# Kernel optimization log

Measured on AMD Instinct MI355X. Metric: run time of the kernel, lower is better.

## Reference

```python
import jax, jax.numpy as jnp
import numpy as np

N, F, H, E, R = 100000, 256, 64, 800000, 7
EPS = 1e-5

def _layernorm(x, g, b):
    mu = jnp.mean(x, axis=-1, keepdims=True)
    var = jnp.mean((x - mu) ** 2, axis=-1, keepdims=True)
    return (x - mu) * jax.lax.rsqrt(var + EPS) * g + b

def setup_inputs() -> dict:
    key = jax.random.key(0)
    ks = jax.random.split(key, 16)
    block_features = jax.random.normal(ks[0], (N, F), dtype=jnp.float32)
    src = jax.random.randint(ks[1], (E,), 0, N).astype(jnp.float32)
    dst = jax.random.randint(ks[2], (E,), 0, N).astype(jnp.float32)
    rel = jax.random.randint(ks[3], (E,), 0, R).astype(jnp.float32)
    w = jax.random.uniform(ks[4], (E,), dtype=jnp.float32)
    typed_edges = jnp.stack([src, dst, rel, w], axis=1)  # [E,4]
    def lin(k, fan_in, fan_out):
        s = 1.0 / np.sqrt(fan_in)
        k1, k2 = jax.random.split(k)
        return (jax.random.uniform(k1, (fan_in, fan_out), jnp.float32, -s, s),
                jax.random.uniform(k2, (fan_out,), jnp.float32, -s, s))
    W1, b1 = lin(ks[5], F, H)
    W2, b2 = lin(ks[6], H, H)
    rel_emb = jax.random.normal(ks[7], (R, H), dtype=jnp.float32)
    Wm1, bm1 = lin(ks[8], 3 * H + 1, H)
    Wm2, bm2 = lin(ks[9], H, H)
    Wg1, bg1 = lin(ks[10], 2 * H, H)
    Wg2, bg2 = lin(ks[11], H, H)
    return dict(block_features=block_features, typed_edges=typed_edges,
                W1=W1, b1=b1, g1=jnp.ones(H), be1=jnp.zeros(H), W2=W2, b2=b2,
                rel_emb=rel_emb, Wm1=Wm1, bm1=bm1, Wm2=Wm2, bm2=bm2,
                gn=jnp.ones(H), bn=jnp.zeros(H), Wg1=Wg1, bg1=bg1, Wg2=Wg2, bg2=bg2)

def reference(block_features, typed_edges, W1, b1, g1, be1, W2, b2, rel_emb,
              Wm1, bm1, Wm2, bm2, gn, bn, Wg1, bg1, Wg2, bg2):
    # node_proj: Linear -> LN -> ReLU -> Linear -> ReLU
    h = jax.nn.relu(_layernorm(block_features @ W1 + b1, g1, be1))
    h = jax.nn.relu(h @ W2 + b2)  # [N,H]
    src = typed_edges[:, 0].astype(jnp.int32)
    dst = typed_edges[:, 1].astype(jnp.int32)
    rel = typed_edges[:, 2].astype(jnp.int32)
    w = typed_edges[:, 3:4]  # [E,1]
    m_in = jnp.concatenate([h[src], h[dst], rel_emb[rel], w], axis=-1)  # [E,3H+1]
    msg = jax.nn.relu(m_in @ Wm1 + bm1) @ Wm2 + bm2  # [E,H]
    agg = jax.ops.segment_sum(msg, dst, num_segments=h.shape[0])  # [N,H]
    nodes = _layernorm(h + agg, gn, bn)
    g = jnp.concatenate([nodes.mean(axis=0), nodes.max(axis=0)], axis=-1)  # [2H]
    return jax.nn.relu(g @ Wg1 + bg1) @ Wg2 + bg2  # [H]
```

## Files before the change

### kernel.cpp

```cpp
#include <hip/hip_runtime.h>

typedef unsigned short u16;
typedef unsigned int   u32;
typedef __attribute__((ext_vector_type(8))) short bf16x8;
typedef __attribute__((ext_vector_type(4))) float f32x4;

#define EPS 1e-5f
#define MFMA(a,b,c) __builtin_amdgcn_mfma_f32_16x16x32_bf16(a,b,c,0,0,0)

constexpr int OB_b1=0, OB_g1=64, OB_be1=128, OB_b2=192, OB_bm1=256, OB_w192=320,
              OB_bm2=384, OB_gn=448, OB_bn=512, OB_bg1=576, OB_bg2=640,
              OB_Wg1=704, OB_Wg2=8896, WB_TOT=12992;
constexpr int FR_Wm1=0;
constexpr int FR_Wm2=12288;
constexpr int FR_rel=16384;
constexpr int FR_W1 =16960;
constexpr int FR_W2 =33344;
constexpr int FR_TOT=37440;

__device__ __forceinline__ float bf2f(u32 u) { return __uint_as_float(u << 16); }
__device__ __forceinline__ u16 f2bf(float f) {
  u32 b = __float_as_uint(f);
  return (u16)((b + 0x7fffu + ((b >> 16) & 1u)) >> 16);
}
__device__ __forceinline__ u32 fkey(float f) {
  u32 b = __float_as_uint(f);
  return (b & 0x80000000u) ? ~b : (b | 0x80000000u);
}

__launch_bounds__(256)
__global__ void k_prep(const float* __restrict__ W1, const float* __restrict__ b1,
                       const float* __restrict__ g1, const float* __restrict__ be1,
                       const float* __restrict__ W2, const float* __restrict__ b2,
                       const float* __restrict__ rel_emb,
                       const float* __restrict__ Wm1, const float* __restrict__ bm1,
                       const float* __restrict__ Wm2, const float* __restrict__ bm2,
                       const float* __restrict__ gn, const float* __restrict__ bn,
                       const float* __restrict__ Wg1, const float* __restrict__ bg1,
                       const float* __restrict__ Wg2, const float* __restrict__ bg2,
                       float* __restrict__ wbuf, u16* __restrict__ frags) {
  int tid = blockIdx.x * 256 + threadIdx.x;
  int nth = gridDim.x * 256;
  for (int i = tid; i < 64; i += nth) {
    wbuf[OB_b1 + i] = b1[i];   wbuf[OB_g1 + i] = g1[i];
    wbuf[OB_be1 + i] = be1[i]; wbuf[OB_b2 + i] = b2[i];
    wbuf[OB_bm1 + i] = bm1[i]; wbuf[OB_w192 + i] = Wm1[192 * 64 + i];
    wbuf[OB_bm2 + i] = bm2[i]; wbuf[OB_gn + i] = gn[i];
    wbuf[OB_bn + i] = bn[i];   wbuf[OB_bg1 + i] = bg1[i];
    wbuf[OB_bg2 + i] = bg2[i];
  }
  for (int i = tid; i < 8192; i += nth) wbuf[OB_Wg1 + i] = Wg1[i];
  for (int i = tid; i < 4096; i += nth) wbuf[OB_Wg2 + i] = Wg2[i];
  for (int idx = tid; idx < 16384; idx += nth) {
    int f = idx >> 9, L = (idx >> 3) & 63, j = idx & 7;
    int k = (f >> 2) * 32 + ((L >> 4) << 3) + j, n = ((f & 3) << 4) + (L & 15);
    frags[FR_W1 + idx] = f2bf(W1[k * 64 + n]);
  }
  for (int idx = tid; idx < 4096; idx += nth) {
    int f = idx >> 9, L = (idx >> 3) & 63, j = idx & 7;
    int k = (f >> 2) * 32 + ((L >> 4) << 3) + j, n = ((f & 3) << 4) + (L & 15);
    frags[FR_W2 + idx] = f2bf(W2[k * 64 + n]);
  }
  for (int idx = tid; idx < 12288; idx += nth) {
    int f = idx >> 9, L = (idx >> 3) & 63, j = idx & 7;
    int k = (f >> 2) * 32 + ((L >> 4) << 3) + j, n = ((f & 3) << 4) + (L & 15);
    frags[FR_Wm1 + idx] = f2bf(Wm1[k * 64 + n]);
  }
  for (int idx = tid; idx < 4096; idx += nth) {
    int f = idx >> 9, L = (idx >> 3) & 63, j = idx & 7;
    int k = (f >> 2) * 32 + ((L >> 4) << 3) + j, n = ((f & 3) << 4) + (L & 15);
    frags[FR_Wm2 + idx] = f2bf(Wm2[k * 64 + n]);
  }
  for (int idx = tid; idx < 576; idx += nth) {
    int r = idx / 80, c = idx % 80;
    frags[FR_rel + idx] = (r < 7 && c < 64) ? f2bf(rel_emb[r * 64 + c]) : (u16)0;
  }
}

__launch_bounds__(256, 3)
__global__ void k_h(const float* __restrict__ X, const float* __restrict__ wbuf,
                    const u16* __restrict__ frags, u16* __restrict__ hb, int N) {
  __shared__ __align__(16) u16 sW1[32 * 512];
  __shared__ __align__(16) u16 sW2[8 * 512];
  __shared__ __align__(16) u16 st[4][16 * 72];

  {
    const uint4* srcp = (const uint4*)(frags + FR_W1);
    uint4* d1 = (uint4*)sW1;
    for (int i = threadIdx.x; i < 2048; i += 256) d1[i] = srcp[i];
    const uint4* srcp2 = (const uint4*)(frags + FR_W2);
    uint4* d2 = (uint4*)sW2;
    for (int i = threadIdx.x; i < 512; i += 256) d2[i] = srcp2[i];
  }
  __syncthreads();

  int lane = threadIdx.x & 63, wave = threadIdx.x >> 6;
  int m = lane & 15, quad = lane >> 4, koff = quad * 8, col0 = m;

  float b1v[4], g1v[4], be1v[4], b2v[4];
  #pragma unroll
  for (int nt = 0; nt < 4; nt++) {
    int c = nt * 16 + col0;
    b1v[nt] = wbuf[OB_b1 + c]; g1v[nt] = wbuf[OB_g1 + c];
    be1v[nt] = wbuf[OB_be1 + c]; b2v[nt] = wbuf[OB_b2 + c];
  }

  int ntiles = (N + 15) / 16;
  int wid = blockIdx.x * 4 + wave, nw = gridDim.x * 4;
  for (int tile = wid; tile < ntiles; tile += nw) {
    int n0 = tile * 16;
    int nm = min(n0 + m, N - 1);
    const float* xr = X + (size_t)nm * 256 + koff;

    f32x4 acc[4] = {};
    #pragma unroll 1
    for (int ks = 0; ks < 8; ks++) {
      float4 u0 = *(const float4*)(xr + ks * 32);
      float4 u1 = *(const float4*)(xr + ks * 32 + 4);
      bf16x8 a;
      a[0] = (short)f2bf(u0.x); a[1] = (short)f2bf(u0.y);
      a[2] = (short)f2bf(u0.z); a[3] = (short)f2bf(u0.w);
      a[4] = (short)f2bf(u1.x); a[5] = (short)f2bf(u1.y);
      a[6] = (short)f2bf(u1.z); a[7] = (short)f2bf(u1.w);
      #pragma unroll
      for (int nt = 0; nt < 4; nt++) {
        bf16x8 b = *(const bf16x8*)(sW1 + (ks * 4 + nt) * 512 + lane * 8);
        acc[nt] = MFMA(a, b, acc[nt]);
      }
    }

    float v[4][4];
    #pragma unroll
    for (int nt = 0; nt < 4; nt++)
      #pragma unroll
      for (int r = 0; r < 4; r++) v[nt][r] = acc[nt][r] + b1v[nt];

    #pragma unroll
    for (int r = 0; r < 4; r++) {
      float s = v[0][r] + v[1][r] + v[2][r] + v[3][r];
      #pragma unroll
      for (int mk = 8; mk >= 1; mk >>= 1) s += __shfl_xor(s, mk, 64);
      float mu = s * (1.f / 64.f);
      float q = 0.f;
      #pragma unroll
      for (int nt = 0; nt < 4; nt++) { float d = v[nt][r] - mu; q += d * d; }
      #pragma unroll
      for (int mk = 8; mk >= 1; mk >>= 1) q += __shfl_xor(q, mk, 64);
      float rs = rsqrtf(q * (1.f / 64.f) + EPS);
      #pragma unroll
      for (int nt = 0; nt < 4; nt++) {
        float h1 = fmaxf(fmaf((v[nt][r] - mu) * rs, g1v[nt], be1v[nt]), 0.f);
        st[wave][(quad * 4 + r) * 72 + nt * 16 + col0] = f2bf(h1);
      }
    }
    __builtin_amdgcn_wave_barrier();

    f32x4 acc2[4] = {};
    #pragma unroll
    for (int ks = 0; ks < 2; ks++) {
      bf16x8 a2 = *(const bf16x8*)(st[wave] + m * 72 + ks * 32 + koff);
      #pragma unroll
      for (int nt = 0; nt < 4; nt++) {
        bf16x8 b = *(const bf16x8*)(sW2 + (ks * 4 + nt) * 512 + lane * 8);
        acc2[nt] = MFMA(a2, b, acc2[nt]);
      }
    }
    __builtin_amdgcn_wave_barrier();

    #pragma unroll
    for (int nt = 0; nt < 4; nt++)
      #pragma unroll
      for (int r = 0; r < 4; r++) {
        int row = n0 + quad * 4 + r;
        if (row < N)
          hb[(size_t)row * 64 + nt * 16 + col0] = f2bf(fmaxf(acc2[nt][r] + b2v[nt], 0.f));
      }
  }
}

__launch_bounds__(512, 6)
__global__ void k_edge(const float* __restrict__ te, const u16* __restrict__ hb,
                       const float* __restrict__ wbuf, const u16* __restrict__ frags,
                       float* __restrict__ agg, int E, int N) {
  __shared__ __align__(16) u16 sWm1[24 * 512];
  __shared__ __align__(16) u16 sWm2[8 * 512];
  __shared__ __align__(16) u16 srel[576];
  __shared__ __align__(16) u16 st[8][16 * 72];

  {
    const uint4* s1 = (const uint4*)(frags + FR_Wm1);
    uint4* d1 = (uint4*)sWm1;
    for (int i = threadIdx.x; i < 1536; i += 512) d1[i] = s1[i];
    const uint4* s2 = (const uint4*)(frags + FR_Wm2);
    uint4* d2 = (uint4*)sWm2;
    for (int i = threadIdx.x; i < 512; i += 512) d2[i] = s2[i];
    const uint4* s3 = (const uint4*)(frags + FR_rel);
    uint4* d3 = (uint4*)srel;
    for (int i = threadIdx.x; i < 72; i += 512) d3[i] = s3[i];
  }
  __syncthreads();

  int lane = threadIdx.x & 63, wave = threadIdx.x >> 6;
  int m = lane & 15, quad = lane >> 4, koff = quad * 8, col0 = m;

  float bm1v[4], w192v[4], bm2v[4];
  #pragma unroll
  for (int nt = 0; nt < 4; nt++) {
    int c = nt * 16 + col0;
    bm1v[nt] = wbuf[OB_bm1 + c];
    w192v[nt] = wbuf[OB_w192 + c];
    bm2v[nt] = wbuf[OB_bm2 + c];
  }

  int ntiles = (E + 15) / 16;
  int wid = blockIdx.x * 8 + wave, nw = gridDim.x * 8;

  int tile = wid;
  int src = 0, dstv = 0, rel = 0; float w = 0.f;
  bf16x8 af[6];

  if (tile < ntiles) {
    if (lane < 16) {
      int e = min(tile * 16 + lane, E - 1);
      float4 v = *(const float4*)(te + (size_t)e * 4);
      src  = min(max((int)v.x, 0), N - 1);
      dstv = min(max((int)v.y, 0), N - 1);
      rel  = min(max((int)v.z, 0), 6);
      w = v.w;
    }
    int sm = __shfl(src, m, 64), dm = __shfl(dstv, m, 64), rm = __shfl(rel, m, 64);
    const u16* hs = hb + (size_t)sm * 64;
    const u16* hd = hb + (size_t)dm * 64;
    af[0] = *(const bf16x8*)(hs + koff);
    af[1] = *(const bf16x8*)(hs + 32 + koff);
    af[2] = *(const bf16x8*)(hd + koff);
    af[3] = *(const bf16x8*)(hd + 32 + koff);
    af[4] = *(const bf16x8*)(srel + rm * 80 + koff);
    af[5] = *(const bf16x8*)(srel + rm * 80 + 32 + koff);
  }

  while (tile < ntiles) {
    int e0 = tile * 16;
    int tile_n = tile + nw;

    f32x4 acc[4] = {};
    #pragma unroll
    for (int ks = 0; ks < 6; ks++)
      #pragma unroll
      for (int nt = 0; nt < 4; nt++) {
        bf16x8 b = *(const bf16x8*)(sWm1 + (ks * 4 + nt) * 512 + lane * 8);
        acc[nt] = MFMA(af[ks], b, acc[nt]);
      }

    int dstc = dstv; float wc = w;

    if (tile_n < ntiles) {
      if (lane < 16) {
        int e = min(tile_n * 16 + lane, E - 1);
        float4 v = *(const float4*)(te + (size_t)e * 4);
        src  = min(max((int)v.x, 0), N - 1);
        dstv = min(max((int)v.y, 0), N - 1);
        rel  = min(max((int)v.z, 0), 6);
        w = v.w;
      }
      int sm = __shfl(src, m, 64), dm = __shfl(dstv, m, 64), rm = __shfl(rel, m, 64);
      const u16* hs = hb + (size_t)sm * 64;
      const u16* hd = hb + (size_t)dm * 64;
      af[0] = *(const bf16x8*)(hs + koff);
      af[1] = *(const bf16x8*)(hs + 32 + koff);
      af[2] = *(const bf16x8*)(hd + koff);
      af[3] = *(const bf16x8*)(hd + 32 + koff);
      af[4] = *(const bf16x8*)(srel + rm * 80 + koff);
      af[5] = *(const bf16x8*)(srel + rm * 80 + 32 + koff);
    }

    float wrow[4];
    #pragma unroll
    for (int r = 0; r < 4; r++) wrow[r] = __shfl(wc, quad * 4 + r, 64);
    #pragma unroll
    for (int nt = 0; nt < 4; nt++)
      #pragma unroll
      for (int r = 0; r < 4; r++) {
        float v = fmaf(wrow[r], w192v[nt], acc[nt][r] + bm1v[nt]);
        st[wave][(quad * 4 + r) * 72 + nt * 16 + col0] = f2bf(fmaxf(v, 0.f));
      }
    __builtin_amdgcn_wave_barrier();

    f32x4 acc2[4] = {};
    #pragma unroll
    for (int ks = 0; ks < 2; ks++) {
      bf16x8 a2 = *(const bf16x8*)(st[wave] + m * 72 + ks * 32 + koff);
      #pragma unroll
      for (int nt = 0; nt < 4; nt++) {
        bf16x8 b = *(const bf16x8*)(sWm2 + (ks * 4 + nt) * 512 + lane * 8);
        acc2[nt] = MFMA(a2, b, acc2[nt]);
      }
    }
    __builtin_amdgcn_wave_barrier();

    #pragma unroll
    for (int r = 0; r < 4; r++) {
      int row = quad * 4 + r;
      int dr = __shfl(dstc, row, 64);
      if (e0 + row < E) {
        #pragma unroll
        for (int nt = 0; nt < 4; nt++)
          atomicAdd(agg + (size_t)dr * 64 + nt * 16 + col0, acc2[nt][r] + bm2v[nt]);
      }
    }

    tile = tile_n;
  }
}

__launch_bounds__(256)
__global__ void k_nodes(const u16* __restrict__ hb, const float* __restrict__ agg,
                        const float* __restrict__ wbuf, float* __restrict__ gsum,
                        u32* __restrict__ gmax, int N) {
  int lane = threadIdx.x & 63, wave = threadIdx.x >> 6;
  int wid = blockIdx.x * 4 + wave;
  int nw = gridDim.x * 4;
  float gn = wbuf[OB_gn + lane], bn = wbuf[OB_bn + lane];
  float sj = 0.f, mj = -3.0e38f;
  for (int n = wid; n < N; n += nw) {
    float v = bf2f(hb[(size_t)n * 64 + lane]) + agg[(size_t)n * 64 + lane];
    float s = v;
    #pragma unroll
    for (int m = 32; m >= 1; m >>= 1) s += __shfl_xor(s, m, 64);
    float mu = s * (1.f / 64.f);
    float d = v - mu;
    float q = d * d;
    #pragma unroll
    for (int m = 32; m >= 1; m >>= 1) q += __shfl_xor(q, m, 64);
    float rs = rsqrtf(q * (1.f / 64.f) + EPS);
    float val = fmaf(d * rs, gn, bn);
    sj += val;
    mj = fmaxf(mj, val);
  }
  __shared__ float bs[256], bm[256];
  bs[threadIdx.x] = sj;
  bm[threadIdx.x] = mj;
  __syncthreads();
  if (threadIdx.x < 64) {
    int t = threadIdx.x;
    float ts = bs[t] + bs[64 + t] + bs[128 + t] + bs[192 + t];
    float tm = fmaxf(fmaxf(bm[t], bm[64 + t]), fmaxf(bm[128 + t], bm[192 + t]));
    atomicAdd(gsum + t, ts);
    atomicMax(gmax + t, fkey(tm));
  }
}

__launch_bounds__(128)
__global__ void k_final(const float* __restrict__ wbuf, const float* __restrict__ gsum,
                        const u32* __restrict__ gmax, float* __restrict__ out, int N) {
  __shared__ float g[128];
  __shared__ float y1[64];
  int t = threadIdx.x;
  if (t < 64) {
    g[t] = gsum[t] / (float)N;
  } else {
    u32 k = gmax[t - 64];
    u32 b = (k & 0x80000000u) ? (k & 0x7fffffffu) : ~k;
    g[t] = __uint_as_float(b);
  }
  __syncthreads();
  if (t < 64) {
    float a = wbuf[OB_bg1 + t];
    for (int i = 0; i < 128; i++) a = fmaf(g[i], wbuf[OB_Wg1 + i * 64 + t], a);
    y1[t] = fmaxf(a, 0.f);
  }
  __syncthreads();
  if (t < 64) {
    float a = wbuf[OB_bg2 + t];
    for (int k = 0; k < 64; k++) a = fmaf(y1[k], wbuf[OB_Wg2 + k * 64 + t], a);
    out[t] = a;
  }
}

extern "C" void kernel_launch(void* const* d_in, const int* in_sizes, int n_in,
                              void* d_out, int out_size, void* d_ws, size_t ws_size,
                              hipStream_t stream) {
  const int N = in_sizes[0] / 256;
  const int E = in_sizes[1] / 4;

  char* ws = (char*)d_ws;
  size_t aggB = (size_t)N * 64 * 4;
  size_t hbB  = (size_t)N * 64 * 2;
  float* agg   = (float*)ws;
  u16*   hb    = (u16*)(ws + aggB);
  float* gsum  = (float*)(ws + aggB + hbB);
  u32*   gmax  = (u32*)(ws + aggB + hbB + 256);
  float* wbuf  = (float*)(ws + aggB + hbB + 512);
  u16*   frags = (u16*)(ws + aggB + hbB + 512 + (size_t)WB_TOT * 4);

  const float* X  = (const float*)d_in[0];
  const float* te = (const float*)d_in[1];

  hipLaunchKernelGGL(k_prep, dim3(64), dim3(256), 0, stream,
                     (const float*)d_in[2], (const float*)d_in[3], (const float*)d_in[4],
                     (const float*)d_in[5], (const float*)d_in[6], (const float*)d_in[7],
                     (const float*)d_in[8], (const float*)d_in[9], (const float*)d_in[10],
                     (const float*)d_in[11], (const float*)d_in[12], (const float*)d_in[13],
                     (const float*)d_in[14], (const float*)d_in[15], (const float*)d_in[16],
                     (const float*)d_in[17], (const float*)d_in[18], wbuf, frags);
  hipMemsetAsync(agg, 0, aggB, stream);
  hipMemsetAsync(gsum, 0, 512, stream);
  hipLaunchKernelGGL(k_h, dim3(640), dim3(256), 0, stream, X, wbuf, frags, hb, N);
  hipLaunchKernelGGL(k_edge, dim3(768), dim3(512), 0, stream, te, hb, wbuf, frags, agg, E, N);
  hipLaunchKernelGGL(k_nodes, dim3(2048), dim3(256), 0, stream, hb, agg, wbuf, gsum, gmax, N);
  hipLaunchKernelGGL(k_final, dim3(1), dim3(128), 0, stream, wbuf, gsum, gmax, (float*)d_out, N);
}
```

Baseline: 452.1 us.

## Sort edges by destination with counting sort and fuse aggregation with node layernorm

Adds a histogram, a three-pass prefix scan and a scatter step that build a destination-sorted (CSR-like) edge list. The edge MLP kernel then assigns 64 destination nodes to each block, accumulates messages in shared memory instead of with global float atomics, and applies the node layernorm and global mean/max pooling in the same kernel. This removes the global agg buffer, its memset and the separate node kernel, at the cost of several extra launches, global atomics in the counting sort, an extra pass over the edges, and load imbalance across blocks with uneven in-degree.

```diff
diff --git a/kernel.cpp b/kernel.cpp
--- a/kernel.cpp
+++ b/kernel.cpp
@@ -77,6 +77,85 @@
   }
 }
 
+__launch_bounds__(256)
+__global__ void k_hist(const float* __restrict__ te, int* __restrict__ cnt, int E, int N) {
+  int i = blockIdx.x * 256 + threadIdx.x, st = gridDim.x * 256;
+  for (int e = i; e < E; e += st) {
+    float4 v = *(const float4*)(te + (size_t)e * 4);
+    int d = min(max((int)v.y, 0), N - 1);
+    atomicAdd(&cnt[d], 1);
+  }
+}
+
+#define SCH 512
+__launch_bounds__(256)
+__global__ void k_scan1(const int* __restrict__ cnt, int* __restrict__ bsum, int N) {
+  __shared__ int sd[256];
+  int b = blockIdx.x, t = threadIdx.x, base = b * SCH;
+  int i0 = base + 2 * t, i1 = i0 + 1;
+  int a = 0;
+  if (i0 < N) a += cnt[i0];
+  if (i1 < N) a += cnt[i1];
+  sd[t] = a; __syncthreads();
+  for (int s = 128; s > 0; s >>= 1) { if (t < s) sd[t] += sd[t + s]; __syncthreads(); }
+  if (t == 0) bsum[b] = sd[0];
+}
+
+__launch_bounds__(256)
+__global__ void k_scan2(const int* __restrict__ bsum, int* __restrict__ bofs,
+                        int* __restrict__ ofs, int NBLK, int N) {
+  __shared__ int sd[256];
+  int t = threadIdx.x;
+  int K = (NBLK + 255) / 256;
+  int loc = 0;
+  for (int k = 0; k < K; k++) { int i = t * K + k; if (i < NBLK) loc += bsum[i]; }
+  sd[t] = loc; __syncthreads();
+  for (int s = 1; s < 256; s <<= 1) {
+    int o = 0; if (t >= s) o = sd[t - s];
+    __syncthreads(); sd[t] += o; __syncthreads();
+  }
+  int excl = sd[t] - loc;
+  int run = excl;
+  for (int k = 0; k < K; k++) {
+    int i = t * K + k;
+    if (i < NBLK) { bofs[i] = run; run += bsum[i]; }
+  }
+  if (t == 255) ofs[N] = sd[255];
+}
+
+__launch_bounds__(256)
+__global__ void k_scan3(const int* __restrict__ bofs, int* __restrict__ ofs,
+                        int* __restrict__ cur, int N) {
+  __shared__ int sd[256];
+  int b = blockIdx.x, t = threadIdx.x, base = b * SCH;
+  int i0 = base + 2 * t, i1 = i0 + 1;
+  int a0 = (i0 < N) ? cur[i0] : 0, a1 = (i1 < N) ? cur[i1] : 0;
+  int pair = a0 + a1;
+  sd[t] = pair; __syncthreads();
+  for (int s = 1; s < 256; s <<= 1) {
+    int o = 0; if (t >= s) o = sd[t - s];
+    __syncthreads(); sd[t] += o; __syncthreads();
+  }
+  int excl = sd[t] - pair + bofs[b];
+  if (i0 < N) { ofs[i0] = excl;      cur[i0] = excl; }
+  if (i1 < N) { ofs[i1] = excl + a0; cur[i1] = excl + a0; }
+}
+
+__launch_bounds__(256)
+__global__ void k_place(const float* __restrict__ te, int* __restrict__ cur,
+                        uint4* __restrict__ sorted, int E, int N) {
+  int i = blockIdx.x * 256 + threadIdx.x, st = gridDim.x * 256;
+  for (int e = i; e < E; e += st) {
+    float4 v = *(const float4*)(te + (size_t)e * 4);
+    int s = min(max((int)v.x, 0), N - 1);
+    int d = min(max((int)v.y, 0), N - 1);
+    int r = min(max((int)v.z, 0), 6);
+    int pos = atomicAdd(&cur[d], 1);
+    uint4 rec; rec.x = (u32)s; rec.y = (u32)d; rec.z = (u32)r; rec.w = __float_as_uint(v.w);
+    sorted[pos] = rec;
+  }
+}
+
 __launch_bounds__(256, 3)
 __global__ void k_h(const float* __restrict__ X, const float* __restrict__ wbuf,
                     const u16* __restrict__ frags, u16* __restrict__ hb, int N) {
@@ -178,14 +257,19 @@
   }
 }
 
-__launch_bounds__(512, 6)
-__global__ void k_edge(const float* __restrict__ te, const u16* __restrict__ hb,
-                       const float* __restrict__ wbuf, const u16* __restrict__ frags,
-                       float* __restrict__ agg, int E, int N) {
+#define DPB 64
+#define APAD 68
+__launch_bounds__(512, 4)
+__global__ void k_edge_agg(const uint4* __restrict__ sorted, const u16* __restrict__ hb,
+                           const float* __restrict__ wbuf, const u16* __restrict__ frags,
+                           const int* __restrict__ ofs,
+                           float* __restrict__ gsum, u32* __restrict__ gmax, int N) {
   __shared__ __align__(16) u16 sWm1[24 * 512];
   __shared__ __align__(16) u16 sWm2[8 * 512];
   __shared__ __align__(16) u16 srel[576];
   __shared__ __align__(16) u16 st[8][16 * 72];
+  __shared__ float accum[DPB * APAD];
+  __shared__ float bs[512], bm[512];
 
   {
     const uint4* s1 = (const uint4*)(frags + FR_Wm1);
@@ -198,10 +282,15 @@
     uint4* d3 = (uint4*)srel;
     for (int i = threadIdx.x; i < 72; i += 512) d3[i] = s3[i];
   }
+  for (int i = threadIdx.x; i < DPB * APAD; i += 512) accum[i] = 0.f;
   __syncthreads();
 
   int lane = threadIdx.x & 63, wave = threadIdx.x >> 6;
   int m = lane & 15, quad = lane >> 4, koff = quad * 8, col0 = m;
+
+  int dlo = blockIdx.x * DPB;
+  int ndst = min(DPB, N - dlo);
+  int elo = ofs[dlo], ehi = ofs[dlo + ndst];
 
   float bm1v[4], w192v[4], bm2v[4];
   #pragma unroll
@@ -212,36 +301,26 @@
     bm2v[nt] = wbuf[OB_bm2 + c];
   }
 
-  int ntiles = (E + 15) / 16;
-  int wid = blockIdx.x * 8 + wave, nw = gridDim.x * 8;
-
-  int tile = wid;
-  int src = 0, dstv = 0, rel = 0; float w = 0.f;
-  bf16x8 af[6];
-
-  if (tile < ntiles) {
+  int ntile = (ehi - elo + 15) >> 4;
+  for (int ti = wave; ti < ntile; ti += 8) {
+    int e0 = elo + ti * 16;
+    int src = 0, dstv = 0, rel = 0; float w = 0.f;
     if (lane < 16) {
-      int e = min(tile * 16 + lane, E - 1);
-      float4 v = *(const float4*)(te + (size_t)e * 4);
-      src  = min(max((int)v.x, 0), N - 1);
-      dstv = min(max((int)v.y, 0), N - 1);
-      rel  = min(max((int)v.z, 0), 6);
-      w = v.w;
+      int e = min(e0 + lane, ehi - 1);
+      uint4 rc = sorted[e];
+      src = (int)rc.x; dstv = (int)rc.y; rel = (int)rc.z; w = __uint_as_float(rc.w);
     }
     int sm = __shfl(src, m, 64), dm = __shfl(dstv, m, 64), rm = __shfl(rel, m, 64);
+
     const u16* hs = hb + (size_t)sm * 64;
     const u16* hd = hb + (size_t)dm * 64;
+    bf16x8 af[6];
     af[0] = *(const bf16x8*)(hs + koff);
     af[1] = *(const bf16x8*)(hs + 32 + koff);
     af[2] = *(const bf16x8*)(hd + koff);
     af[3] = *(const bf16x8*)(hd + 32 + koff);
     af[4] = *(const bf16x8*)(srel + rm * 80 + koff);
     af[5] = *(const bf16x8*)(srel + rm * 80 + 32 + koff);
-  }
-
-  while (tile < ntiles) {
-    int e0 = tile * 16;
-    int tile_n = tile + nw;
 
     f32x4 acc[4] = {};
     #pragma unroll
@@ -252,31 +331,9 @@
         acc[nt] = MFMA(af[ks], b, acc[nt]);
       }
 
-    int dstc = dstv; float wc = w;
-
-    if (tile_n < ntiles) {
-      if (lane < 16) {
-        int e = min(tile_n * 16 + lane, E - 1);
-        float4 v = *(const float4*)(te + (size_t)e * 4);
-        src  = min(max((int)v.x, 0), N - 1);
-        dstv = min(max((int)v.y, 0), N - 1);
-        rel  = min(max((int)v.z, 0), 6);
-        w = v.w;
-      }
-      int sm = __shfl(src, m, 64), dm = __shfl(dstv, m, 64), rm = __shfl(rel, m, 64);
-      const u16* hs = hb + (size_t)sm * 64;
-      const u16* hd = hb + (size_t)dm * 64;
-      af[0] = *(const bf16x8*)(hs + koff);
-      af[1] = *(const bf16x8*)(hs + 32 + koff);
-      af[2] = *(const bf16x8*)(hd + koff);
-      af[3] = *(const bf16x8*)(hd + 32 + koff);
-      af[4] = *(const bf16x8*)(srel + rm * 80 + koff);
-      af[5] = *(const bf16x8*)(srel + rm * 80 + 32 + koff);
-    }
-
     float wrow[4];
     #pragma unroll
-    for (int r = 0; r < 4; r++) wrow[r] = __shfl(wc, quad * 4 + r, 64);
+    for (int r = 0; r < 4; r++) wrow[r] = __shfl(w, quad * 4 + r, 64);
     #pragma unroll
     for (int nt = 0; nt < 4; nt++)
       #pragma unroll
@@ -301,50 +358,49 @@
     #pragma unroll
     for (int r = 0; r < 4; r++) {
       int row = quad * 4 + r;
-      int dr = __shfl(dstc, row, 64);
-      if (e0 + row < E) {
+      if (e0 + row < ehi) {
+        int dr = __shfl(dstv, row, 64) - dlo;
         #pragma unroll
         for (int nt = 0; nt < 4; nt++)
-          atomicAdd(agg + (size_t)dr * 64 + nt * 16 + col0, acc2[nt][r] + bm2v[nt]);
-      }
-    }
-
-    tile = tile_n;
-  }
-}
-
-__launch_bounds__(256)
-__global__ void k_nodes(const u16* __restrict__ hb, const float* __restrict__ agg,
-                        const float* __restrict__ wbuf, float* __restrict__ gsum,
-                        u32* __restrict__ gmax, int N) {
-  int lane = threadIdx.x & 63, wave = threadIdx.x >> 6;
-  int wid = blockIdx.x * 4 + wave;
-  int nw = gridDim.x * 4;
-  float gn = wbuf[OB_gn + lane], bn = wbuf[OB_bn + lane];
+          atomicAdd(&accum[dr * APAD + nt * 16 + col0], acc2[nt][r] + bm2v[nt]);
+      }
+    }
+  }
+  __syncthreads();
+
+  float gnv = wbuf[OB_gn + lane], bnv = wbuf[OB_bn + lane];
   float sj = 0.f, mj = -3.0e38f;
-  for (int n = wid; n < N; n += nw) {
-    float v = bf2f(hb[(size_t)n * 64 + lane]) + agg[(size_t)n * 64 + lane];
-    float s = v;
-    #pragma unroll
-    for (int m = 32; m >= 1; m >>= 1) s += __shfl_xor(s, m, 64);
-    float mu = s * (1.f / 64.f);
-    float d = v - mu;
-    float q = d * d;
-    #pragma unroll
-    for (int m = 32; m >= 1; m >>= 1) q += __shfl_xor(q, m, 64);
-    float rs = rsqrtf(q * (1.f / 64.f) + EPS);
-    float val = fmaf(d * rs, gn, bn);
-    sj += val;
-    mj = fmaxf(mj, val);
-  }
-  __shared__ float bs[256], bm[256];
+  #pragma unroll
+  for (int k = 0; k < 8; k++) {
+    int rr = wave * 8 + k;
+    if (rr < ndst) {
+      int nrow = dlo + rr;
+      float v = bf2f(hb[(size_t)nrow * 64 + lane]) + accum[rr * APAD + lane];
+      float s = v;
+      #pragma unroll
+      for (int mk = 32; mk >= 1; mk >>= 1) s += __shfl_xor(s, mk, 64);
+      float mu = s * (1.f / 64.f);
+      float d = v - mu;
+      float q = d * d;
+      #pragma unroll
+      for (int mk = 32; mk >= 1; mk >>= 1) q += __shfl_xor(q, mk, 64);
+      float rs = rsqrtf(q * (1.f / 64.f) + EPS);
+      float val = fmaf(d * rs, gnv, bnv);
+      sj += val;
+      mj = fmaxf(mj, val);
+    }
+  }
   bs[threadIdx.x] = sj;
   bm[threadIdx.x] = mj;
   __syncthreads();
   if (threadIdx.x < 64) {
     int t = threadIdx.x;
-    float ts = bs[t] + bs[64 + t] + bs[128 + t] + bs[192 + t];
-    float tm = fmaxf(fmaxf(bm[t], bm[64 + t]), fmaxf(bm[128 + t], bm[192 + t]));
+    float ts = 0.f, tm = -3.0e38f;
+    #pragma unroll
+    for (int wv = 0; wv < 8; wv++) {
+      ts += bs[wv * 64 + t];
+      tm = fmaxf(tm, bm[wv * 64 + t]);
+    }
     atomicAdd(gsum + t, ts);
     atomicMax(gmax + t, fkey(tm));
   }
@@ -382,16 +438,21 @@
                               hipStream_t stream) {
   const int N = in_sizes[0] / 256;
   const int E = in_sizes[1] / 4;
+  const int NBLK = (N + SCH - 1) / SCH;
 
   char* ws = (char*)d_ws;
-  size_t aggB = (size_t)N * 64 * 4;
-  size_t hbB  = (size_t)N * 64 * 2;
-  float* agg   = (float*)ws;
-  u16*   hb    = (u16*)(ws + aggB);
-  float* gsum  = (float*)(ws + aggB + hbB);
-  u32*   gmax  = (u32*)(ws + aggB + hbB + 256);
-  float* wbuf  = (float*)(ws + aggB + hbB + 512);
-  u16*   frags = (u16*)(ws + aggB + hbB + 512 + (size_t)WB_TOT * 4);
+  size_t p = 0;
+  auto rup = [](size_t x) { return (x + 255) & ~(size_t)255; };
+  uint4* sorted = (uint4*)(ws + p); p += rup((size_t)E * 16);
+  u16*   hb     = (u16*)(ws + p);   p += rup((size_t)N * 128);
+  int*   ofs    = (int*)(ws + p);   p += rup((size_t)(N + 1) * 4);
+  int*   cur    = (int*)(ws + p);   p += rup((size_t)N * 4);
+  int*   bsum   = (int*)(ws + p);   p += rup((size_t)(NBLK + 1) * 4);
+  int*   bofs   = (int*)(ws + p);   p += rup((size_t)(NBLK + 1) * 4);
+  float* gsum   = (float*)(ws + p); p += 256;
+  u32*   gmax   = (u32*)(ws + p);   p += 256;
+  float* wbuf   = (float*)(ws + p); p += rup((size_t)WB_TOT * 4);
+  u16*   frags  = (u16*)(ws + p);   p += rup((size_t)FR_TOT * 2);
 
   const float* X  = (const float*)d_in[0];
   const float* te = (const float*)d_in[1];
@@ -403,10 +464,19 @@
                      (const float*)d_in[11], (const float*)d_in[12], (const float*)d_in[13],
                      (const float*)d_in[14], (const float*)d_in[15], (const float*)d_in[16],
                      (const float*)d_in[17], (const float*)d_in[18], wbuf, frags);
-  hipMemsetAsync(agg, 0, aggB, stream);
-  hipMemsetAsync(gsum, 0, 512, stream);
+  hipMemsetAsync(cur, 0, (size_t)N * 4, stream);
+  hipMemsetAsync(gsum, 0, 256, stream);
+  hipMemsetAsync(gmax, 0, 256, stream);
+
+  hipLaunchKernelGGL(k_hist, dim3(1024), dim3(256), 0, stream, te, cur, E, N);
+  hipLaunchKernelGGL(k_scan1, dim3(NBLK), dim3(256), 0, stream, cur, bsum, N);
+  hipLaunchKernelGGL(k_scan2, dim3(1), dim3(256), 0, stream, bsum, bofs, ofs, NBLK, N);
+  hipLaunchKernelGGL(k_scan3, dim3(NBLK), dim3(256), 0, stream, bofs, ofs, cur, N);
+
   hipLaunchKernelGGL(k_h, dim3(640), dim3(256), 0, stream, X, wbuf, frags, hb, N);
-  hipLaunchKernelGGL(k_edge, dim3(768), dim3(512), 0, stream, te, hb, wbuf, frags, agg, E, N);
-  hipLaunchKernelGGL(k_nodes, dim3(2048), dim3(256), 0, stream, hb, agg, wbuf, gsum, gmax, N);
+  hipLaunchKernelGGL(k_place, dim3(1024), dim3(256), 0, stream, te, cur, sorted, E, N);
+
+  hipLaunchKernelGGL(k_edge_agg, dim3((N + DPB - 1) / DPB), dim3(512), 0, stream,
+                     sorted, hb, wbuf, frags, ofs, gsum, gmax, N);
   hipLaunchKernelGGL(k_final, dim3(1), dim3(128), 0, stream, wbuf, gsum, gmax, (float*)d_out, N);
 }
```

After: 652.1 us. 44.2% more time.
